# Kernel optimization log

Measured on AMD Instinct MI355X. Metric: run time of the kernel, lower is better.

Reference implementation:

```python
import jax, jax.numpy as jnp
import numpy as np

B, S, D, H = 4, 1024, 1024, 16
DEPTH = D // H


def setup_inputs() -> dict:
    key = jax.random.key(0)
    ks = jax.random.split(key, 13)
    inp = {
        'query': jax.random.normal(ks[0], (B, S, D), dtype=jnp.float32),
        'key': jax.random.normal(ks[1], (B, S, D), dtype=jnp.float32),
        'value': jax.random.normal(ks[2], (B, S, D), dtype=jnp.float32),
        'mask': jax.random.bernoulli(ks[3], 0.1, (B, S, S)),
    }
    scale = 1.0 / np.sqrt(D)
    inp['wq_w'] = jax.random.uniform(ks[4], (D, D), jnp.float32, -scale, scale)
    inp['wq_b'] = jax.random.uniform(ks[5], (D,), jnp.float32, -scale, scale)
    inp['wk_w'] = jax.random.uniform(ks[6], (D, D), jnp.float32, -scale, scale)
    inp['wk_b'] = jax.random.uniform(ks[7], (D,), jnp.float32, -scale, scale)
    inp['wv_w'] = jax.random.uniform(ks[8], (D, D), jnp.float32, -scale, scale)
    inp['wv_b'] = jax.random.uniform(ks[9], (D,), jnp.float32, -scale, scale)
    inp['fc_w'] = jax.random.uniform(ks[10], (D, D), jnp.float32, -scale, scale)
    inp['fc_b'] = jax.random.uniform(ks[11], (D,), jnp.float32, -scale, scale)
    return inp


def _split_heads(x):
    # [B,S,D] -> [B,H,S,depth]
    b, s, _ = x.shape
    return x.reshape(b, s, H, DEPTH).transpose(0, 2, 1, 3)


def reference(query, key, value, mask, wq_w, wq_b, wk_w, wk_b, wv_w, wv_b, fc_w, fc_b):
    q = _split_heads(query @ wq_w.T + wq_b)
    k = _split_heads(key @ wk_w.T + wk_b)
    v = _split_heads(value @ wv_w.T + wv_b)
    scores = jnp.einsum('bhqd,bhkd->bhqk', q, k) / jnp.sqrt(jnp.float32(DEPTH))
    scores = jnp.where(mask[:, None, :, :], jnp.float32(-1e9), scores)
    attn = jax.nn.softmax(scores, axis=-1)
    out = jnp.einsum('bhqk,bhkd->bhqd', attn, v)  # [B,H,S,depth]
    out = out.transpose(0, 2, 1, 3).reshape(query.shape[0], -1, D)
    return out @ fc_w.T + fc_b
```

## Files before the change

kernel.cpp:

```cpp
#include <hip/hip_runtime.h>
#include <hip/hip_bf16.h>


typedef __bf16 bf16x8 __attribute__((ext_vector_type(8)));
typedef __bf16 bf16x4 __attribute__((ext_vector_type(4)));
typedef float  f32x4  __attribute__((ext_vector_type(4)));
typedef float  f32x16 __attribute__((ext_vector_type(16)));

typedef const __attribute__((address_space(1))) void* gptr_t;
typedef __attribute__((address_space(3))) void* lptr_t;

#define MFMA16(a, b, c) __builtin_amdgcn_mfma_f32_16x16x32_bf16((a), (b), (c), 0, 0, 0)
#define MFMA32(a, b, c) __builtin_amdgcn_mfma_f32_32x32x16_bf16((a), (b), (c), 0, 0, 0)

__device__ __forceinline__ void gload_lds16(const void* g, void* l) {
  __builtin_amdgcn_global_load_lds((gptr_t)g, (lptr_t)l, 16, 0, 0);
}

__device__ __forceinline__ unsigned pack2(float a, float b) {
  union { __bf16 h[2]; unsigned u; } x;
  x.h[0] = (__bf16)a; x.h[1] = (__bf16)b; return x.u;
}

__device__ __forceinline__ bf16x8 mkfrag(unsigned a, unsigned b, unsigned c, unsigned d) {
  union { unsigned w[4]; bf16x8 v; } x;
  x.w[0] = a; x.w[1] = b; x.w[2] = c; x.w[3] = d; return x.v;
}

__global__ void detect_mask(const unsigned char* m, int* flag) {
  __shared__ int s1[4], s23[4];
  int tid = threadIdx.x;
  uint4 v = ((const uint4*)m)[tid];
  unsigned x0 = v.x, x1 = v.y, x2 = v.z, x3 = v.w;
  unsigned c1  = (x0 & 0x0000ff00u) | (x1 & 0x0000ff00u) | (x2 & 0x0000ff00u) | (x3 & 0x0000ff00u);
  unsigned c23 = (x0 & 0xffff0000u) | (x1 & 0xffff0000u) | (x2 & 0xffff0000u) | (x3 & 0xffff0000u);
  unsigned long long b1 = __ballot(c1 != 0), b23 = __ballot(c23 != 0);
  if ((tid & 63) == 0) { s1[tid >> 6] = (b1 != 0); s23[tid >> 6] = (b23 != 0); }
  __syncthreads();
  if (tid == 0) {
    int a1 = s1[0] | s1[1] | s1[2] | s1[3];
    int a23 = s23[0] | s23[1] | s23[2] | s23[3];
    *flag = a1 ? 1 : (a23 ? 2 : 0);
  }
}

__global__ void pack_mask(const void* m, const int* flag, unsigned int* out) {
  size_t i = (size_t)blockIdx.x * 256 + threadIdx.x;
  int f = *flag;
  bool v;
  if (f == 1)      v = ((const unsigned char*)m)[i] != 0;
  else if (f == 2) v = ((const float*)m)[i] != 0.0f;
  else             v = ((const int*)m)[i] != 0;
  unsigned long long bal = __ballot(v);
  int lane = threadIdx.x & 63;
  if ((lane & 31) == 0) out[i >> 5] = (unsigned int)(bal >> (lane & 32));
}

__global__ void cvt3(const float* a, const float* b, const float* c,
                     __bf16* oa, __bf16* ob, __bf16* oc) {
  int bid = blockIdx.x;
  int which = bid >> 12, sub = bid & 4095;
  const float* in = which == 0 ? a : which == 1 ? b : c;
  __bf16* out = which == 0 ? oa : which == 1 ? ob : oc;
  size_t i = (size_t)sub * 256 + threadIdx.x;
  float4 v = ((const float4*)in)[i];
  bf16x4 o; o[0] = (__bf16)v.x; o[1] = (__bf16)v.y; o[2] = (__bf16)v.z; o[3] = (__bf16)v.w;
  ((bf16x4*)out)[i] = o;
}

__global__ void cvt4(const float* a, const float* b, const float* c, const float* d,
                     __bf16* oa, __bf16* ob, __bf16* oc, __bf16* od) {
  int bid = blockIdx.x;
  int which = bid >> 10, sub = bid & 1023;
  const float* in = which == 0 ? a : which == 1 ? b : which == 2 ? c : d;
  __bf16* out = which == 0 ? oa : which == 1 ? ob : which == 2 ? oc : od;
  size_t i = (size_t)sub * 256 + threadIdx.x;
  float4 v = ((const float4*)in)[i];
  bf16x4 o; o[0] = (__bf16)v.x; o[1] = (__bf16)v.y; o[2] = (__bf16)v.z; o[3] = (__bf16)v.w;
  ((bf16x4*)out)[i] = o;
}

__global__ __launch_bounds__(256, 2)
void gemm_qkv(const __bf16* qb, const __bf16* kb, const __bf16* vb,
              const __bf16* wq, const __bf16* wk, const __bf16* wv,
              const float* bq, const float* bk, const float* bv,
              __bf16* Qp, __bf16* Kp, __bf16* Vt) {
  __shared__ __bf16 As[128 * 64];
  __shared__ __bf16 Bs[128 * 64];
  const int bm = blockIdx.x;
  const int bnall = blockIdx.y;
  const int which = bnall >> 3;
  const int bn = bnall & 7;
  const __bf16* A = which == 0 ? qb : which == 1 ? kb : vb;
  const __bf16* W = which == 0 ? wq : which == 1 ? wk : wv;
  const float* bias = which == 0 ? bq : which == 1 ? bk : bv;

  const int tid = threadIdx.x, wave = tid >> 6, lane = tid & 63;
  const int wr = wave >> 1, wc = wave & 1;
  const int rl = lane >> 3, c8 = lane & 7;
  f32x4 acc[4][4] = {};

  for (int kt = 0; kt < 16; ++kt) {
    __syncthreads();
#pragma unroll
    for (int i = 0; i < 4; ++i) {
      int row = wave * 32 + i * 8 + rl;
      int sw = (c8 ^ (row & 7)) << 3;
      gload_lds16(A + (size_t)(bm * 128 + row) * 1024 + kt * 64 + sw, As + (wave * 32 + i * 8) * 64);
      gload_lds16(W + (size_t)(bn * 128 + row) * 1024 + kt * 64 + sw, Bs + (wave * 32 + i * 8) * 64);
    }
    __syncthreads();
#pragma unroll
    for (int k32 = 0; k32 < 2; ++k32) {
      bf16x8 af[4], bfr[4];
#pragma unroll
      for (int mi = 0; mi < 4; ++mi) {
        int row = wr * 64 + mi * 16 + (lane & 15);
        af[mi] = *(const bf16x8*)(As + row * 64 + (((k32 * 4 + (lane >> 4)) ^ (row & 7)) << 3));
      }
#pragma unroll
      for (int ni = 0; ni < 4; ++ni) {
        int row = wc * 64 + ni * 16 + (lane & 15);
        bfr[ni] = *(const bf16x8*)(Bs + row * 64 + (((k32 * 4 + (lane >> 4)) ^ (row & 7)) << 3));
      }
#pragma unroll
      for (int mi = 0; mi < 4; ++mi)
#pragma unroll
        for (int ni = 0; ni < 4; ++ni)
          acc[mi][ni] = MFMA16(af[mi], bfr[ni], acc[mi][ni]);
    }
  }
  const int r0 = (lane >> 4) * 4, cl = lane & 15;
  __bf16* Onat = which == 0 ? Qp : Kp;
#pragma unroll
  for (int ni = 0; ni < 4; ++ni) {
    int col = bn * 128 + wc * 64 + ni * 16 + cl;
    float bvv = bias[col];
#pragma unroll
    for (int mi = 0; mi < 4; ++mi) {
      int rowb = bm * 128 + wr * 64 + mi * 16 + r0;
      if (which < 2) {
#pragma unroll
        for (int r = 0; r < 4; ++r)
          Onat[(size_t)(rowb + r) * 1024 + col] = (__bf16)(acc[mi][ni][r] + bvv);
      } else {
        int bb = rowb >> 10, s0 = rowb & 1023, hh = col >> 6, d = col & 63;
        bf16x4 ov;
#pragma unroll
        for (int r = 0; r < 4; ++r) ov[r] = (__bf16)(acc[mi][ni][r] + bvv);
        *(bf16x4*)(Vt + (((size_t)(bb * 16 + hh) * 64 + d) << 10) + s0) = ov;
      }
    }
  }
}

__global__ __launch_bounds__(256, 2)
void gemm_fc(const __bf16* A, const __bf16* W, const float* bias, float* C) {
  __shared__ __bf16 As[128 * 64];
  __shared__ __bf16 Bs[128 * 64];
  const int bm = blockIdx.x, bn = blockIdx.y;
  const int tid = threadIdx.x, wave = tid >> 6, lane = tid & 63;
  const int wr = wave >> 1, wc = wave & 1;
  const int rl = lane >> 3, c8 = lane & 7;
  f32x4 acc[4][4] = {};

  for (int kt = 0; kt < 16; ++kt) {
    __syncthreads();
#pragma unroll
    for (int i = 0; i < 4; ++i) {
      int row = wave * 32 + i * 8 + rl;
      int sw = (c8 ^ (row & 7)) << 3;
      gload_lds16(A + (size_t)(bm * 128 + row) * 1024 + kt * 64 + sw, As + (wave * 32 + i * 8) * 64);
      gload_lds16(W + (size_t)(bn * 128 + row) * 1024 + kt * 64 + sw, Bs + (wave * 32 + i * 8) * 64);
    }
    __syncthreads();
#pragma unroll
    for (int k32 = 0; k32 < 2; ++k32) {
      bf16x8 af[4], bfr[4];
#pragma unroll
      for (int mi = 0; mi < 4; ++mi) {
        int row = wr * 64 + mi * 16 + (lane & 15);
        af[mi] = *(const bf16x8*)(As + row * 64 + (((k32 * 4 + (lane >> 4)) ^ (row & 7)) << 3));
      }
#pragma unroll
      for (int ni = 0; ni < 4; ++ni) {
        int row = wc * 64 + ni * 16 + (lane & 15);
        bfr[ni] = *(const bf16x8*)(Bs + row * 64 + (((k32 * 4 + (lane >> 4)) ^ (row & 7)) << 3));
      }
#pragma unroll
      for (int mi = 0; mi < 4; ++mi)
#pragma unroll
        for (int ni = 0; ni < 4; ++ni)
          acc[mi][ni] = MFMA16(af[mi], bfr[ni], acc[mi][ni]);
    }
  }
  const int r0 = (lane >> 4) * 4, cl = lane & 15;
#pragma unroll
  for (int ni = 0; ni < 4; ++ni) {
    int col = bn * 128 + wc * 64 + ni * 16 + cl;
    float bvv = bias[col];
#pragma unroll
    for (int mi = 0; mi < 4; ++mi) {
      int rowb = bm * 128 + wr * 64 + mi * 16 + r0;
#pragma unroll
      for (int r = 0; r < 4; ++r)
        C[(size_t)(rowb + r) * 1024 + col] = acc[mi][ni][r] + bvv;
    }
  }
}

__global__ __launch_bounds__(256)
void attn32(const __bf16* __restrict__ Qp, const __bf16* __restrict__ Kp,
            const __bf16* __restrict__ Vt, const unsigned long long* __restrict__ mp64,
            __bf16* __restrict__ O) {
  const int tid = threadIdx.x, wave = tid >> 6, lane = tid & 63;
  const int lo5 = lane & 31, hi = lane >> 5;
  const int bx = blockIdx.x;
  const int qt = bx & 7, h = (bx >> 3) & 15, b = bx >> 7;
  const int qrow = qt * 128 + wave * 32 + lo5;
  const float SC = 0.18033688011112042f;

  bf16x8 qf[4];
  const __bf16* qb = Qp + ((size_t)(b * 1024 + qrow)) * 1024 + h * 64 + hi * 8;
#pragma unroll
  for (int m = 0; m < 4; ++m) qf[m] = *(const bf16x8*)(qb + m * 16);

  f32x16 oacc0 = {}, oacc1 = {};
  float dsum = 0.0f;
  const unsigned long long* mrow = mp64 + ((size_t)(b * 1024 + qrow)) * 16;
  const __bf16* vrow = Vt + ((size_t)((b * 16 + h) * 64 + lo5)) * 1024;

  for (int kt = 0; kt < 16; ++kt) {
    unsigned long long mw = mrow[kt];
    const __bf16* kb = Kp + ((size_t)(b * 1024 + kt * 64 + lo5)) * 1024 + h * 64 + hi * 8;
    const __bf16* vb = vrow + kt * 64 + hi * 8;

    f32x16 s0 = {};
#pragma unroll
    for (int m = 0; m < 4; ++m)
      s0 = MFMA32(*(const bf16x8*)(kb + m * 16), qf[m], s0);
    float p0[16];
#pragma unroll
    for (int r = 0; r < 16; ++r) {
      int cr = (r & 3) + 8 * (r >> 2) + 4 * hi;
      float e = exp2f(s0[r] * SC);
      p0[r] = ((mw >> cr) & 1) ? 0.0f : e;
      dsum += p0[r];
    }
    unsigned own0[8], rcv0[8];
#pragma unroll
    for (int u = 0; u < 4; ++u) {
      own0[2 * u]     = pack2(p0[4 * u],     p0[4 * u + 1]);
      own0[2 * u + 1] = pack2(p0[4 * u + 2], p0[4 * u + 3]);
    }
#pragma unroll
    for (int i = 0; i < 8; ++i) rcv0[i] = (unsigned)__shfl_xor((int)own0[i], 32, 64);
#pragma unroll
    for (int s = 0; s < 2; ++s) {
      const int ue2 = 4 * s, uo2 = 4 * s + 2;
      unsigned fw0 = hi ? rcv0[uo2 + 0] : own0[ue2 + 0];
      unsigned fw1 = hi ? rcv0[uo2 + 1] : own0[ue2 + 1];
      unsigned fw2 = hi ? own0[uo2 + 0] : rcv0[ue2 + 0];
      unsigned fw3 = hi ? own0[uo2 + 1] : rcv0[ue2 + 1];
      bf16x8 pa = mkfrag(fw0, fw1, fw2, fw3);
      bf16x8 vf0 = *(const bf16x8*)(vb + s * 16);
      bf16x8 vf1 = *(const bf16x8*)(vb + s * 16 + 32 * 1024);
      oacc0 = MFMA32(pa, vf0, oacc0);
      oacc1 = MFMA32(pa, vf1, oacc1);
    }

    f32x16 s1 = {};
#pragma unroll
    for (int m = 0; m < 4; ++m)
      s1 = MFMA32(*(const bf16x8*)(kb + 32 * 1024 + m * 16), qf[m], s1);
    float p1[16];
#pragma unroll
    for (int r = 0; r < 16; ++r) {
      int cr = (r & 3) + 8 * (r >> 2) + 4 * hi;
      float e = exp2f(s1[r] * SC);
      p1[r] = ((mw >> (32 + cr)) & 1) ? 0.0f : e;
      dsum += p1[r];
    }
    unsigned own1[8], rcv1[8];
#pragma unroll
    for (int u = 0; u < 4; ++u) {
      own1[2 * u]     = pack2(p1[4 * u],     p1[4 * u + 1]);
      own1[2 * u + 1] = pack2(p1[4 * u + 2], p1[4 * u + 3]);
    }
#pragma unroll
    for (int i = 0; i < 8; ++i) rcv1[i] = (unsigned)__shfl_xor((int)own1[i], 32, 64);
#pragma unroll
    for (int s = 0; s < 2; ++s) {
      const int ue2 = 4 * s, uo2 = 4 * s + 2;
      unsigned fw0 = hi ? rcv1[uo2 + 0] : own1[ue2 + 0];
      unsigned fw1 = hi ? rcv1[uo2 + 1] : own1[ue2 + 1];
      unsigned fw2 = hi ? own1[uo2 + 0] : rcv1[ue2 + 0];
      unsigned fw3 = hi ? own1[uo2 + 1] : rcv1[ue2 + 1];
      bf16x8 pa = mkfrag(fw0, fw1, fw2, fw3);
      bf16x8 vf0 = *(const bf16x8*)(vb + (s + 2) * 16);
      bf16x8 vf1 = *(const bf16x8*)(vb + (s + 2) * 16 + 32 * 1024);
      oacc0 = MFMA32(pa, vf0, oacc0);
      oacc1 = MFMA32(pa, vf1, oacc1);
    }
  }

  dsum += __shfl_xor(dsum, 32, 64);
  float inv = 1.0f / dsum;

  const size_t orow0 = (size_t)(b * 1024 + qt * 128 + wave * 32);
#pragma unroll
  for (int r = 0; r < 16; ++r) {
    int cr = (r & 3) + 8 * (r >> 2) + 4 * hi;
    float iv = __shfl(inv, cr, 64);
    __bf16* op = O + (orow0 + cr) * 1024 + h * 64 + lo5;
    op[0]  = (__bf16)(oacc0[r] * iv);
    op[32] = (__bf16)(oacc1[r] * iv);
  }
}

extern "C" void kernel_launch(void* const* d_in, const int* in_sizes, int n_in,
                              void* d_out, int out_size, void* d_ws, size_t ws_size,
                              hipStream_t stream) {
  const float* query = (const float*)d_in[0];
  const float* key   = (const float*)d_in[1];
  const float* value = (const float*)d_in[2];
  const void*  mask  = d_in[3];
  const float* wq_w  = (const float*)d_in[4];
  const float* wq_b  = (const float*)d_in[5];
  const float* wk_w  = (const float*)d_in[6];
  const float* wk_b  = (const float*)d_in[7];
  const float* wv_w  = (const float*)d_in[8];
  const float* wv_b  = (const float*)d_in[9];
  const float* fc_w  = (const float*)d_in[10];
  const float* fc_b  = (const float*)d_in[11];

  char* ws = (char*)d_ws;
  __bf16* qb  = (__bf16*)ws;
  __bf16* kb  = qb  + 4194304;
  __bf16* vb  = kb  + 4194304;
  __bf16* wqb = vb  + 4194304;
  __bf16* wkb = wqb + 1048576;
  __bf16* wvb = wkb + 1048576;
  __bf16* fcb = wvb + 1048576;
  __bf16* Qp  = fcb + 1048576;
  __bf16* Kp  = Qp  + 4194304;
  __bf16* Vt  = Kp  + 4194304;
  __bf16* Ob  = Vt  + 4194304;
  unsigned int* mpk = (unsigned int*)(Ob + 4194304);
  int* flag = (int*)(mpk + 131072);

  detect_mask<<<1, 256, 0, stream>>>((const unsigned char*)mask, flag);
  pack_mask<<<16384, 256, 0, stream>>>(mask, flag, mpk);
  cvt3<<<12288, 256, 0, stream>>>(query, key, value, qb, kb, vb);
  cvt4<<<4096, 256, 0, stream>>>(wq_w, wk_w, wv_w, fc_w, wqb, wkb, wvb, fcb);
  dim3 g1(32, 24);
  gemm_qkv<<<g1, 256, 0, stream>>>(qb, kb, vb, wqb, wkb, wvb, wq_b, wk_b, wv_b, Qp, Kp, Vt);
  attn32<<<512, 256, 0, stream>>>(Qp, Kp, Vt, (const unsigned long long*)mpk, Ob);
  dim3 g2(32, 8);
  gemm_fc<<<g2, 256, 0, stream>>>(Ob, fcb, fc_b, (float*)d_out);
}
```

Baseline: 261.9 us.

## Double-buffer LDS tiles in GEMMs and attention, merge conversion kernels

Both projection GEMMs now use two LDS buffers, so the next K tile's global-to-LDS load is issued before the MFMA work on the current tile, with one barrier per iteration instead of two. The attention kernel now stages K and V tiles through swizzled, double-buffered LDS shared by all four waves, replacing per-wave direct global loads. The two fp32-to-bf16 conversion kernels are merged into one launch. This doubles LDS use per block, which may lower occupancy. Correctness depends on the async LDS loads having completed by the barrier.

```diff
diff --git a/kernel.cpp b/kernel.cpp
--- a/kernel.cpp
+++ b/kernel.cpp
@@ -56,37 +56,37 @@
   if ((lane & 31) == 0) out[i >> 5] = (unsigned int)(bal >> (lane & 32));
 }
 
-__global__ void cvt3(const float* a, const float* b, const float* c,
-                     __bf16* oa, __bf16* ob, __bf16* oc) {
+__global__ void cvt_all(const float* q, const float* k, const float* v,
+                        const float* w0, const float* w1, const float* w2, const float* w3,
+                        __bf16* oq, __bf16* ok, __bf16* ov,
+                        __bf16* o0, __bf16* o1, __bf16* o2, __bf16* o3) {
   int bid = blockIdx.x;
-  int which = bid >> 12, sub = bid & 4095;
-  const float* in = which == 0 ? a : which == 1 ? b : c;
-  __bf16* out = which == 0 ? oa : which == 1 ? ob : oc;
+  const float* in; __bf16* out; int sub;
+  if (bid < 12288) {
+    int w = bid >> 12; sub = bid & 4095;
+    in = w == 0 ? q : w == 1 ? k : v;
+    out = w == 0 ? oq : w == 1 ? ok : ov;
+  } else {
+    int w = (bid - 12288) >> 10; sub = (bid - 12288) & 1023;
+    in = w == 0 ? w0 : w == 1 ? w1 : w == 2 ? w2 : w3;
+    out = w == 0 ? o0 : w == 1 ? o1 : w == 2 ? o2 : o3;
+  }
   size_t i = (size_t)sub * 256 + threadIdx.x;
-  float4 v = ((const float4*)in)[i];
-  bf16x4 o; o[0] = (__bf16)v.x; o[1] = (__bf16)v.y; o[2] = (__bf16)v.z; o[3] = (__bf16)v.w;
+  float4 vv = ((const float4*)in)[i];
+  bf16x4 o; o[0] = (__bf16)vv.x; o[1] = (__bf16)vv.y; o[2] = (__bf16)vv.z; o[3] = (__bf16)vv.w;
   ((bf16x4*)out)[i] = o;
 }
 
-__global__ void cvt4(const float* a, const float* b, const float* c, const float* d,
-                     __bf16* oa, __bf16* ob, __bf16* oc, __bf16* od) {
-  int bid = blockIdx.x;
-  int which = bid >> 10, sub = bid & 1023;
-  const float* in = which == 0 ? a : which == 1 ? b : which == 2 ? c : d;
-  __bf16* out = which == 0 ? oa : which == 1 ? ob : which == 2 ? oc : od;
-  size_t i = (size_t)sub * 256 + threadIdx.x;
-  float4 v = ((const float4*)in)[i];
-  bf16x4 o; o[0] = (__bf16)v.x; o[1] = (__bf16)v.y; o[2] = (__bf16)v.z; o[3] = (__bf16)v.w;
-  ((bf16x4*)out)[i] = o;
-}
-
 __global__ __launch_bounds__(256, 2)
-void gemm_qkv(const __bf16* qb, const __bf16* kb, const __bf16* vb,
-              const __bf16* wq, const __bf16* wk, const __bf16* wv,
-              const float* bq, const float* bk, const float* bv,
-              __bf16* Qp, __bf16* Kp, __bf16* Vt) {
-  __shared__ __bf16 As[128 * 64];
-  __shared__ __bf16 Bs[128 * 64];
+void gemm_qkv(const __bf16* __restrict__ qb, const __bf16* __restrict__ kb,
+              const __bf16* __restrict__ vb,
+              const __bf16* __restrict__ wq, const __bf16* __restrict__ wk,
+              const __bf16* __restrict__ wv,
+              const float* __restrict__ bq, const float* __restrict__ bk,
+              const float* __restrict__ bv,
+              __bf16* __restrict__ Qp, __bf16* __restrict__ Kp, __bf16* __restrict__ Vt) {
+  __shared__ __bf16 As[2][128 * 64];
+  __shared__ __bf16 Bs[2][128 * 64];
   const int bm = blockIdx.x;
   const int bnall = blockIdx.y;
   const int which = bnall >> 3;
@@ -100,28 +100,36 @@
   const int rl = lane >> 3, c8 = lane & 7;
   f32x4 acc[4][4] = {};
 
+#define QKV_STAGE(bb, kt)                                                             \
+  {                                                                                   \
+    _Pragma("unroll")                                                                 \
+    for (int i = 0; i < 4; ++i) {                                                     \
+      int row = wave * 32 + i * 8 + rl;                                               \
+      int sw = (c8 ^ (row & 7)) << 3;                                                 \
+      gload_lds16(A + (size_t)(bm * 128 + row) * 1024 + (kt) * 64 + sw,               \
+                  &As[bb][(wave * 32 + i * 8) * 64]);                                 \
+      gload_lds16(W + (size_t)(bn * 128 + row) * 1024 + (kt) * 64 + sw,               \
+                  &Bs[bb][(wave * 32 + i * 8) * 64]);                                 \
+    }                                                                                 \
+  }
+
+  QKV_STAGE(0, 0);
+  __syncthreads();
+  int buf = 0;
   for (int kt = 0; kt < 16; ++kt) {
-    __syncthreads();
-#pragma unroll
-    for (int i = 0; i < 4; ++i) {
-      int row = wave * 32 + i * 8 + rl;
-      int sw = (c8 ^ (row & 7)) << 3;
-      gload_lds16(A + (size_t)(bm * 128 + row) * 1024 + kt * 64 + sw, As + (wave * 32 + i * 8) * 64);
-      gload_lds16(W + (size_t)(bn * 128 + row) * 1024 + kt * 64 + sw, Bs + (wave * 32 + i * 8) * 64);
-    }
-    __syncthreads();
+    if (kt < 15) QKV_STAGE(buf ^ 1, kt + 1);
 #pragma unroll
     for (int k32 = 0; k32 < 2; ++k32) {
       bf16x8 af[4], bfr[4];
 #pragma unroll
       for (int mi = 0; mi < 4; ++mi) {
         int row = wr * 64 + mi * 16 + (lane & 15);
-        af[mi] = *(const bf16x8*)(As + row * 64 + (((k32 * 4 + (lane >> 4)) ^ (row & 7)) << 3));
+        af[mi] = *(const bf16x8*)(&As[buf][row * 64 + (((k32 * 4 + (lane >> 4)) ^ (row & 7)) << 3)]);
       }
 #pragma unroll
       for (int ni = 0; ni < 4; ++ni) {
         int row = wc * 64 + ni * 16 + (lane & 15);
-        bfr[ni] = *(const bf16x8*)(Bs + row * 64 + (((k32 * 4 + (lane >> 4)) ^ (row & 7)) << 3));
+        bfr[ni] = *(const bf16x8*)(&Bs[buf][row * 64 + (((k32 * 4 + (lane >> 4)) ^ (row & 7)) << 3)]);
       }
 #pragma unroll
       for (int mi = 0; mi < 4; ++mi)
@@ -129,6 +137,8 @@
         for (int ni = 0; ni < 4; ++ni)
           acc[mi][ni] = MFMA16(af[mi], bfr[ni], acc[mi][ni]);
     }
+    __syncthreads();
+    buf ^= 1;
   }
   const int r0 = (lane >> 4) * 4, cl = lane & 15;
   __bf16* Onat = which == 0 ? Qp : Kp;
@@ -155,37 +165,46 @@
 }
 
 __global__ __launch_bounds__(256, 2)
-void gemm_fc(const __bf16* A, const __bf16* W, const float* bias, float* C) {
-  __shared__ __bf16 As[128 * 64];
-  __shared__ __bf16 Bs[128 * 64];
+void gemm_fc(const __bf16* __restrict__ A, const __bf16* __restrict__ W,
+             const float* __restrict__ bias, float* __restrict__ C) {
+  __shared__ __bf16 As[2][128 * 64];
+  __shared__ __bf16 Bs[2][128 * 64];
   const int bm = blockIdx.x, bn = blockIdx.y;
   const int tid = threadIdx.x, wave = tid >> 6, lane = tid & 63;
   const int wr = wave >> 1, wc = wave & 1;
   const int rl = lane >> 3, c8 = lane & 7;
   f32x4 acc[4][4] = {};
 
+#define FC_STAGE(bb, kt)                                                              \
+  {                                                                                   \
+    _Pragma("unroll")                                                                 \
+    for (int i = 0; i < 4; ++i) {                                                     \
+      int row = wave * 32 + i * 8 + rl;                                               \
+      int sw = (c8 ^ (row & 7)) << 3;                                                 \
+      gload_lds16(A + (size_t)(bm * 128 + row) * 1024 + (kt) * 64 + sw,               \
+                  &As[bb][(wave * 32 + i * 8) * 64]);                                 \
+      gload_lds16(W + (size_t)(bn * 128 + row) * 1024 + (kt) * 64 + sw,               \
+                  &Bs[bb][(wave * 32 + i * 8) * 64]);                                 \
+    }                                                                                 \
+  }
+
+  FC_STAGE(0, 0);
+  __syncthreads();
+  int buf = 0;
   for (int kt = 0; kt < 16; ++kt) {
-    __syncthreads();
-#pragma unroll
-    for (int i = 0; i < 4; ++i) {
-      int row = wave * 32 + i * 8 + rl;
-      int sw = (c8 ^ (row & 7)) << 3;
-      gload_lds16(A + (size_t)(bm * 128 + row) * 1024 + kt * 64 + sw, As + (wave * 32 + i * 8) * 64);
-      gload_lds16(W + (size_t)(bn * 128 + row) * 1024 + kt * 64 + sw, Bs + (wave * 32 + i * 8) * 64);
-    }
-    __syncthreads();
+    if (kt < 15) FC_STAGE(buf ^ 1, kt + 1);
 #pragma unroll
     for (int k32 = 0; k32 < 2; ++k32) {
       bf16x8 af[4], bfr[4];
 #pragma unroll
       for (int mi = 0; mi < 4; ++mi) {
         int row = wr * 64 + mi * 16 + (lane & 15);
-        af[mi] = *(const bf16x8*)(As + row * 64 + (((k32 * 4 + (lane >> 4)) ^ (row & 7)) << 3));
+        af[mi] = *(const bf16x8*)(&As[buf][row * 64 + (((k32 * 4 + (lane >> 4)) ^ (row & 7)) << 3)]);
       }
 #pragma unroll
       for (int ni = 0; ni < 4; ++ni) {
         int row = wc * 64 + ni * 16 + (lane & 15);
-        bfr[ni] = *(const bf16x8*)(Bs + row * 64 + (((k32 * 4 + (lane >> 4)) ^ (row & 7)) << 3));
+        bfr[ni] = *(const bf16x8*)(&Bs[buf][row * 64 + (((k32 * 4 + (lane >> 4)) ^ (row & 7)) << 3)]);
       }
 #pragma unroll
       for (int mi = 0; mi < 4; ++mi)
@@ -193,6 +212,8 @@
         for (int ni = 0; ni < 4; ++ni)
           acc[mi][ni] = MFMA16(af[mi], bfr[ni], acc[mi][ni]);
     }
+    __syncthreads();
+    buf ^= 1;
   }
   const int r0 = (lane >> 4) * 4, cl = lane & 15;
 #pragma unroll
@@ -213,6 +234,8 @@
 void attn32(const __bf16* __restrict__ Qp, const __bf16* __restrict__ Kp,
             const __bf16* __restrict__ Vt, const unsigned long long* __restrict__ mp64,
             __bf16* __restrict__ O) {
+  __shared__ __bf16 Ks[2][64 * 64];
+  __shared__ __bf16 Vs[2][64 * 64];
   const int tid = threadIdx.x, wave = tid >> 6, lane = tid & 63;
   const int lo5 = lane & 31, hi = lane >> 5;
   const int bx = blockIdx.x;
@@ -220,6 +243,22 @@
   const int qrow = qt * 128 + wave * 32 + lo5;
   const float SC = 0.18033688011112042f;
 
+  const int srow = tid >> 3;
+  const int sgx = ((tid & 7) ^ (srow & 7)) << 3;
+
+#define ATTN_STAGE(bb, kt)                                                            \
+  {                                                                                   \
+    _Pragma("unroll")                                                                 \
+    for (int i = 0; i < 2; ++i) {                                                     \
+      gload_lds16(Kp + (size_t)(b * 1024 + (kt) * 64 + i * 32 + srow) * 1024          \
+                     + h * 64 + sgx,                                                  \
+                  &Ks[bb][i * 2048 + wave * 512]);                                    \
+      gload_lds16(Vt + (size_t)((b * 16 + h) * 64 + i * 32 + srow) * 1024             \
+                     + (kt) * 64 + sgx,                                               \
+                  &Vs[bb][i * 2048 + wave * 512]);                                    \
+    }                                                                                 \
+  }
+
   bf16x8 qf[4];
   const __bf16* qb = Qp + ((size_t)(b * 1024 + qrow)) * 1024 + h * 64 + hi * 8;
 #pragma unroll
@@ -228,80 +267,55 @@
   f32x16 oacc0 = {}, oacc1 = {};
   float dsum = 0.0f;
   const unsigned long long* mrow = mp64 + ((size_t)(b * 1024 + qrow)) * 16;
-  const __bf16* vrow = Vt + ((size_t)((b * 16 + h) * 64 + lo5)) * 1024;
-
+  const int x = lo5 & 7;
+
+  ATTN_STAGE(0, 0);
+  __syncthreads();
+  int buf = 0;
   for (int kt = 0; kt < 16; ++kt) {
+    if (kt < 15) ATTN_STAGE(buf ^ 1, kt + 1);
     unsigned long long mw = mrow[kt];
-    const __bf16* kb = Kp + ((size_t)(b * 1024 + kt * 64 + lo5)) * 1024 + h * 64 + hi * 8;
-    const __bf16* vb = vrow + kt * 64 + hi * 8;
-
-    f32x16 s0 = {};
-#pragma unroll
-    for (int m = 0; m < 4; ++m)
-      s0 = MFMA32(*(const bf16x8*)(kb + m * 16), qf[m], s0);
-    float p0[16];
-#pragma unroll
-    for (int r = 0; r < 16; ++r) {
-      int cr = (r & 3) + 8 * (r >> 2) + 4 * hi;
-      float e = exp2f(s0[r] * SC);
-      p0[r] = ((mw >> cr) & 1) ? 0.0f : e;
-      dsum += p0[r];
-    }
-    unsigned own0[8], rcv0[8];
-#pragma unroll
-    for (int u = 0; u < 4; ++u) {
-      own0[2 * u]     = pack2(p0[4 * u],     p0[4 * u + 1]);
-      own0[2 * u + 1] = pack2(p0[4 * u + 2], p0[4 * u + 3]);
-    }
-#pragma unroll
-    for (int i = 0; i < 8; ++i) rcv0[i] = (unsigned)__shfl_xor((int)own0[i], 32, 64);
-#pragma unroll
-    for (int s = 0; s < 2; ++s) {
-      const int ue2 = 4 * s, uo2 = 4 * s + 2;
-      unsigned fw0 = hi ? rcv0[uo2 + 0] : own0[ue2 + 0];
-      unsigned fw1 = hi ? rcv0[uo2 + 1] : own0[ue2 + 1];
-      unsigned fw2 = hi ? own0[uo2 + 0] : rcv0[ue2 + 0];
-      unsigned fw3 = hi ? own0[uo2 + 1] : rcv0[ue2 + 1];
-      bf16x8 pa = mkfrag(fw0, fw1, fw2, fw3);
-      bf16x8 vf0 = *(const bf16x8*)(vb + s * 16);
-      bf16x8 vf1 = *(const bf16x8*)(vb + s * 16 + 32 * 1024);
-      oacc0 = MFMA32(pa, vf0, oacc0);
-      oacc1 = MFMA32(pa, vf1, oacc1);
-    }
-
-    f32x16 s1 = {};
-#pragma unroll
-    for (int m = 0; m < 4; ++m)
-      s1 = MFMA32(*(const bf16x8*)(kb + 32 * 1024 + m * 16), qf[m], s1);
-    float p1[16];
-#pragma unroll
-    for (int r = 0; r < 16; ++r) {
-      int cr = (r & 3) + 8 * (r >> 2) + 4 * hi;
-      float e = exp2f(s1[r] * SC);
-      p1[r] = ((mw >> (32 + cr)) & 1) ? 0.0f : e;
-      dsum += p1[r];
-    }
-    unsigned own1[8], rcv1[8];
-#pragma unroll
-    for (int u = 0; u < 4; ++u) {
-      own1[2 * u]     = pack2(p1[4 * u],     p1[4 * u + 1]);
-      own1[2 * u + 1] = pack2(p1[4 * u + 2], p1[4 * u + 3]);
-    }
-#pragma unroll
-    for (int i = 0; i < 8; ++i) rcv1[i] = (unsigned)__shfl_xor((int)own1[i], 32, 64);
-#pragma unroll
-    for (int s = 0; s < 2; ++s) {
-      const int ue2 = 4 * s, uo2 = 4 * s + 2;
-      unsigned fw0 = hi ? rcv1[uo2 + 0] : own1[ue2 + 0];
-      unsigned fw1 = hi ? rcv1[uo2 + 1] : own1[ue2 + 1];
-      unsigned fw2 = hi ? own1[uo2 + 0] : rcv1[ue2 + 0];
-      unsigned fw3 = hi ? own1[uo2 + 1] : rcv1[ue2 + 1];
-      bf16x8 pa = mkfrag(fw0, fw1, fw2, fw3);
-      bf16x8 vf0 = *(const bf16x8*)(vb + (s + 2) * 16);
-      bf16x8 vf1 = *(const bf16x8*)(vb + (s + 2) * 16 + 32 * 1024);
-      oacc0 = MFMA32(pa, vf0, oacc0);
-      oacc1 = MFMA32(pa, vf1, oacc1);
-    }
+#pragma unroll
+    for (int sub = 0; sub < 2; ++sub) {
+      f32x16 s = {};
+#pragma unroll
+      for (int m = 0; m < 4; ++m) {
+        bf16x8 kf = *(const bf16x8*)(&Ks[buf][(sub * 32 + lo5) * 64 + (((2 * m + hi) ^ x) << 3)]);
+        s = MFMA32(kf, qf[m], s);
+      }
+      float p[16];
+#pragma unroll
+      for (int r = 0; r < 16; ++r) {
+        int cr = (r & 3) + 8 * (r >> 2) + 4 * hi;
+        float e = exp2f(s[r] * SC);
+        p[r] = ((mw >> (sub * 32 + cr)) & 1) ? 0.0f : e;
+        dsum += p[r];
+      }
+      unsigned own[8], rcv[8];
+#pragma unroll
+      for (int u = 0; u < 4; ++u) {
+        own[2 * u]     = pack2(p[4 * u],     p[4 * u + 1]);
+        own[2 * u + 1] = pack2(p[4 * u + 2], p[4 * u + 3]);
+      }
+#pragma unroll
+      for (int i = 0; i < 8; ++i) rcv[i] = (unsigned)__shfl_xor((int)own[i], 32, 64);
+#pragma unroll
+      for (int sf = 0; sf < 2; ++sf) {
+        const int ue2 = 4 * sf, uo2 = 4 * sf + 2;
+        unsigned fw0 = hi ? rcv[uo2 + 0] : own[ue2 + 0];
+        unsigned fw1 = hi ? rcv[uo2 + 1] : own[ue2 + 1];
+        unsigned fw2 = hi ? own[uo2 + 0] : rcv[ue2 + 0];
+        unsigned fw3 = hi ? own[uo2 + 1] : rcv[ue2 + 1];
+        bf16x8 pa = mkfrag(fw0, fw1, fw2, fw3);
+        int g = ((sub * 4 + sf * 2 + hi) ^ x) << 3;
+        bf16x8 vf0 = *(const bf16x8*)(&Vs[buf][lo5 * 64 + g]);
+        bf16x8 vf1 = *(const bf16x8*)(&Vs[buf][(lo5 + 32) * 64 + g]);
+        oacc0 = MFMA32(pa, vf0, oacc0);
+        oacc1 = MFMA32(pa, vf1, oacc1);
+      }
+    }
+    __syncthreads();
+    buf ^= 1;
   }
 
   dsum += __shfl_xor(dsum, 32, 64);
@@ -351,8 +365,8 @@
 
   detect_mask<<<1, 256, 0, stream>>>((const unsigned char*)mask, flag);
   pack_mask<<<16384, 256, 0, stream>>>(mask, flag, mpk);
-  cvt3<<<12288, 256, 0, stream>>>(query, key, value, qb, kb, vb);
-  cvt4<<<4096, 256, 0, stream>>>(wq_w, wk_w, wv_w, fc_w, wqb, wkb, wvb, fcb);
+  cvt_all<<<16384, 256, 0, stream>>>(query, key, value, wq_w, wk_w, wv_w, fc_w,
+                                     qb, kb, vb, wqb, wkb, wvb, fcb);
   dim3 g1(32, 24);
   gemm_qkv<<<g1, 256, 0, stream>>>(qb, kb, vb, wqb, wkb, wvb, wq_b, wk_b, wv_b, Qp, Kp, Vt);
   attn32<<<512, 256, 0, stream>>>(Qp, Kp, Vt, (const unsigned long long*)mpk, Ob);
```

New measurement: 248.3 us. -5.2%, faster.
